# Optimization experiments

Measured on AMD Instinct MI355X. Metric: run time of the kernel, lower is better.

Reference implementation:

```python
import jax, jax.numpy as jnp
import numpy as np

SCALE = 0.05  # temperature from the module
C, NUM, IN_DIM, HID = 64, 128, 768, 128


def _l2norm(x):
    n = jnp.sqrt(jnp.sum(x * x, axis=-1, keepdims=True))
    return x / jnp.maximum(n, 1e-12)


def setup_inputs() -> dict:
    key = jax.random.key(0)
    k1, k2, k3, k4 = jax.random.split(key, 4)
    embeds = jax.random.normal(k1, (C, NUM, IN_DIM), dtype=jnp.float32)
    head_w = jax.random.normal(k2, (HID, IN_DIM), dtype=jnp.float32) * (1.0 / np.sqrt(IN_DIM))
    head_b = jax.random.normal(k3, (HID,), dtype=jnp.float32) * 0.01
    proto = jax.random.normal(k4, (C, HID), dtype=jnp.float32) * (1.0 / np.sqrt(HID))
    return {"embeds": embeds, "head_w": head_w, "head_b": head_b, "proto": proto}


def reference(embeds, head_w, head_b, proto):
    # x = head(embeds): [C, num, hid]
    x = jnp.einsum('cni,hi->cnh', embeds, head_w) + head_b
    num = x.shape[1]
    num_classes = proto.shape[0]

    nx = _l2norm(x)            # [C, num, d]
    nproto = _l2norm(proto)    # [C, d]

    # ---- prototype contrastive term (loop over i in num, fused) ----
    # sim_mat[c, n, k] = exp(cos(x[c,n], proto[k]) / scale)
    sim_mat = jnp.exp(jnp.einsum('cnd,kd->cnk', nx, nproto) / SCALE)
    pos = jnp.diagonal(sim_mat, axis1=0, axis2=2)      # [num, C], pos[n,c] = sim_mat[c,n,c]
    total = sim_mat.sum(-1).T                           # [num, C]
    loss = -jnp.log(pos / total).sum()
    loss = loss / (num * num_classes * num_classes)

    # ---- instance-instance term (loop over i in num_classes, fused) ----
    # S[a, m, b, n] = exp(cos(x[a,m], x[b,n]) / scale)
    S = jnp.exp(jnp.einsum('amd,bnd->ambn', nx, nx) / SCALE)
    # per-anchor-class i: pos_ins[m, n] = S[i, m, i, n]
    pos_ins = jnp.diagonal(S, axis1=0, axis2=2)         # [m, n, C(i)]
    sumA = jnp.transpose(S.sum(0), (0, 2, 1))           # [m, n, C(i)]
    neg_ins = (sumA - pos_ins).sum(0)                   # [n, C(i)]
    loss_ins = -jnp.log(pos_ins / (pos_ins + neg_ins[None, :, :])).sum()
    loss_ins = loss_ins / (num * num_classes * num * num_classes)

    return loss + loss_ins
```

## Files before the change

### kernel.cpp

```cpp
#include <hip/hip_runtime.h>
#include <math.h>

#define SCALE_INV 20.0f
#define EXPK 28.853900817779268f
#define LN2F 0.6931471805599453f

typedef __bf16 bf16x8 __attribute__((ext_vector_type(8)));
typedef float  f32x4  __attribute__((ext_vector_type(4)));

__global__ __launch_bounds__(256) void k_prep(const float* __restrict__ w,
                                              const float* __restrict__ proto,
                                              __bf16* __restrict__ wb,
                                              __bf16* __restrict__ nprE,
                                              float* __restrict__ accs) {
  const int b = blockIdx.x, t = threadIdx.x;
  if (b < 32) {
    __shared__ float wsum[4];
    const int sub = t >> 7, tt = t & 127, row = b * 2 + sub;
    float v = proto[row * 128 + tt];
    float s = v * v;
    for (int off = 32; off; off >>= 1) s += __shfl_xor(s, off, 64);
    if ((t & 63) == 0) wsum[t >> 6] = s;
    __syncthreads();
    float inv = 1.0f / fmaxf(sqrtf(wsum[sub * 2] + wsum[sub * 2 + 1]), 1e-12f);
    nprE[row * 128 + tt] = (__bf16)(v * inv * EXPK);
    if (b == 0 && t < 4) accs[t] = 0.0f;
  } else {
    int i = (b - 32) * 1024 + t * 4;
    float4 f = *(const float4*)&w[i];
    __bf16 o[4] = {(__bf16)f.x, (__bf16)f.y, (__bf16)f.z, (__bf16)f.w};
    *(float*)&wb[i] = *(float*)o;
  }
}

__global__ __launch_bounds__(256) void k_headnorm(const float* __restrict__ e,
                                                  const __bf16* __restrict__ wb,
                                                  const float* __restrict__ hb,
                                                  __bf16* __restrict__ nxb,
                                                  __bf16* __restrict__ nxe) {
  __shared__ __bf16 Ab[32 * 136];
  __shared__ __bf16 Bb[128 * 136];
  __shared__ float  xt[32 * 132];
  __shared__ float  hbl[128];
  const int t  = threadIdx.x;
  const int rt = blockIdx.x;
  if (t < 128) hbl[t] = hb[t];

  const int arow = t >> 3, akoff = (t & 7) * 16;
  const int brow = t >> 1, bkoff = (t & 1) * 64;
  float4 ar[4];
  bf16x8 brg[8];
  {
    const float* p = &e[(rt * 32 + arow) * 768 + akoff];
    for (int i = 0; i < 4; i++) ar[i] = *(const float4*)(p + 4 * i);
    const __bf16* q = &wb[brow * 768 + bkoff];
    for (int i = 0; i < 8; i++) brg[i] = *(const bf16x8*)(q + 8 * i);
  }

  const int wv = t >> 6, lane = t & 63;
  const int quad = lane >> 4, lrow = lane & 15;
  const int rb = wv & 1, cb = wv >> 1;
  f32x4 acc[4];
  f32x4 zero = {0.f, 0.f, 0.f, 0.f};
  for (int j = 0; j < 4; j++) acc[j] = zero;

  for (int it = 0; it < 6; it++) {
    {
      __bf16 ta[16];
      const float* f = (const float*)ar;
      for (int i = 0; i < 16; i++) ta[i] = (__bf16)f[i];
      *(bf16x8*)&Ab[arow * 136 + akoff]     = *(bf16x8*)ta;
      *(bf16x8*)&Ab[arow * 136 + akoff + 8] = *(bf16x8*)(ta + 8);
      for (int seg = 0; seg < 8; seg++)
        *(bf16x8*)&Bb[brow * 136 + bkoff + seg * 8] = brg[seg];
    }
    __syncthreads();
    if (it < 5) {
      int kb = (it + 1) * 128;
      const float* p = &e[(rt * 32 + arow) * 768 + kb + akoff];
      for (int i = 0; i < 4; i++) ar[i] = *(const float4*)(p + 4 * i);
      const __bf16* q = &wb[brow * 768 + kb + bkoff];
      for (int i = 0; i < 8; i++) brg[i] = *(const bf16x8*)(q + 8 * i);
    }
    for (int kc = 0; kc < 4; kc++) {
      bf16x8 a = *(const bf16x8*)&Ab[(rb * 16 + lrow) * 136 + kc * 32 + quad * 8];
      for (int j = 0; j < 4; j++) {
        bf16x8 b = *(const bf16x8*)&Bb[(cb * 64 + j * 16 + lrow) * 136 + kc * 32 + quad * 8];
        acc[j] = __builtin_amdgcn_mfma_f32_16x16x32_bf16(a, b, acc[j], 0, 0, 0);
      }
    }
    __syncthreads();
  }

  for (int j = 0; j < 4; j++)
    for (int r = 0; r < 4; r++) {
      int row = rb * 16 + quad * 4 + r;
      int col = cb * 64 + j * 16 + lrow;
      xt[row * 132 + col] = acc[j][r] + hbl[col];
    }
  __syncthreads();
  {
    int row = t >> 3, c0 = (t & 7) * 16;
    float v[16];
    float s = 0.0f;
    for (int i = 0; i < 4; i++) {
      float4 f = *(const float4*)&xt[row * 132 + c0 + i * 4];
      v[i * 4] = f.x; v[i * 4 + 1] = f.y; v[i * 4 + 2] = f.z; v[i * 4 + 3] = f.w;
    }
    for (int i = 0; i < 16; i++) s += v[i] * v[i];
    s += __shfl_xor(s, 1, 64);
    s += __shfl_xor(s, 2, 64);
    s += __shfl_xor(s, 4, 64);
    float inv = 1.0f / fmaxf(sqrtf(s), 1e-12f);
    __bf16 o[16], oe[16];
    for (int i = 0; i < 16; i++) {
      float nv = v[i] * inv;
      o[i]  = (__bf16)nv;
      oe[i] = (__bf16)(nv * EXPK);
    }
    __bf16* dst = &nxb[(rt * 32 + row) * 128 + c0];
    *(bf16x8*)dst       = *(bf16x8*)o;
    *(bf16x8*)(dst + 8) = *(bf16x8*)(o + 8);
    __bf16* dse = &nxe[(rt * 32 + row) * 128 + c0];
    *(bf16x8*)dse       = *(bf16x8*)oe;
    *(bf16x8*)(dse + 8) = *(bf16x8*)(oe + 8);
  }
}

__global__ __launch_bounds__(256) void k_colsum(const __bf16* __restrict__ nxb,
                                                const __bf16* __restrict__ nxe,
                                                float* __restrict__ cspart) {
  __shared__ __bf16 At[128 * 136];
  __shared__ __bf16 Bt[128 * 136];
  __shared__ float  colpart[4 * 128];
  const int t    = threadIdx.x;
  const int ct   = blockIdx.x;
  const int rs   = blockIdx.y;
  const int w    = t >> 6, lane = t & 63;
  const int quad = lane >> 4, lrow = lane & 15;
  const int sr   = t >> 4, sseg = t & 15;

  for (int it = 0; it < 8; it++) {
    int r = sr + it * 16;
    *(bf16x8*)&Bt[r * 136 + sseg * 8] =
        *(const bf16x8*)&nxe[(ct * 128 + r) * 128 + sseg * 8];
  }
  int tiles[8], nt = 0;
  for (int c8 = 0; c8 < 8; c8++) {
    int row0 = rs * 1024 + c8 * 128;
    if (row0 != ct * 128) tiles[nt++] = row0;
  }
  bf16x8 pre[8];
  for (int it = 0; it < 8; it++)
    pre[it] = *(const bf16x8*)&nxb[(tiles[0] + sr + it * 16) * 128 + sseg * 8];

  float colacc[8];
  for (int j = 0; j < 8; j++) colacc[j] = 0.0f;

  for (int ti = 0; ti < nt; ti++) {
    for (int it = 0; it < 8; it++)
      *(bf16x8*)&At[(sr + it * 16) * 136 + sseg * 8] = pre[it];
    __syncthreads();
    if (ti + 1 < nt) {
      int row0 = tiles[ti + 1];
      for (int it = 0; it < 8; it++)
        pre[it] = *(const bf16x8*)&nxb[(row0 + sr + it * 16) * 128 + sseg * 8];
    }
    f32x4 acc[2][8];
    f32x4 zero = {0.0f, 0.0f, 0.0f, 0.0f};
    for (int i = 0; i < 2; i++)
      for (int j = 0; j < 8; j++) acc[i][j] = zero;
    for (int kc = 0; kc < 4; kc++) {
      bf16x8 a0 = *(const bf16x8*)&At[(w * 32 + lrow) * 136 + kc * 32 + quad * 8];
      bf16x8 a1 = *(const bf16x8*)&At[(w * 32 + 16 + lrow) * 136 + kc * 32 + quad * 8];
      for (int j = 0; j < 8; j++) {
        bf16x8 b = *(const bf16x8*)&Bt[(j * 16 + lrow) * 136 + kc * 32 + quad * 8];
        acc[0][j] = __builtin_amdgcn_mfma_f32_16x16x32_bf16(a0, b, acc[0][j], 0, 0, 0);
        acc[1][j] = __builtin_amdgcn_mfma_f32_16x16x32_bf16(a1, b, acc[1][j], 0, 0, 0);
      }
    }
    for (int i = 0; i < 2; i++)
      for (int j = 0; j < 8; j++)
        for (int r = 0; r < 4; r++)
          colacc[j] += exp2f(acc[i][j][r]);
    __syncthreads();
  }

  for (int j = 0; j < 8; j++) {
    float v = colacc[j];
    v += __shfl_xor(v, 16, 64);
    v += __shfl_xor(v, 32, 64);
    if (lane < 16) colpart[w * 128 + j * 16 + lane] = v;
  }
  __syncthreads();
  if (t < 128) {
    float s = colpart[t] + colpart[128 + t] + colpart[256 + t] + colpart[384 + t];
    cspart[rs * 8192 + ct * 128 + t] = s;
  }
}

__global__ __launch_bounds__(256) void k_fused(const __bf16* __restrict__ nxb,
                                               const __bf16* __restrict__ nxe,
                                               const __bf16* __restrict__ nprE,
                                               const float* __restrict__ cspart,
                                               float* __restrict__ accs,
                                               float* __restrict__ out) {
  __shared__ __bf16 Xt[64 * 136];
  __shared__ __bf16 XtE[128 * 136];
  __shared__ __bf16 PtE[64 * 136];
  __shared__ float  negl[128];
  const int t = threadIdx.x, cls = blockIdx.x, half = blockIdx.y;
  const int sr = t >> 4, sseg = t & 15;

  for (int it = 0; it < 4; it++) {
    int r = sr + it * 16;
    *(bf16x8*)&Xt[r * 136 + sseg * 8] =
        *(const bf16x8*)&nxb[(cls * 128 + half * 64 + r) * 128 + sseg * 8];
    *(bf16x8*)&PtE[r * 136 + sseg * 8] =
        *(const bf16x8*)&nprE[r * 128 + sseg * 8];
  }
  for (int it = 0; it < 8; it++) {
    int r = sr + it * 16;
    *(bf16x8*)&XtE[r * 136 + sseg * 8] =
        *(const bf16x8*)&nxe[(cls * 128 + r) * 128 + sseg * 8];
  }
  if (t < 128) {
    float s = 0.0f;
    for (int s8 = 0; s8 < 8; s8++) s += cspart[s8 * 8192 + cls * 128 + t];
    negl[t] = s;
  }
  __syncthreads();

  const int wv = t >> 6, lane = t & 63;
  const int quad = lane >> 4, lrow = lane & 15;
  f32x4 zero = {0.f, 0.f, 0.f, 0.f};
  f32x4 acc_i[8], acc_p[4];
  for (int j = 0; j < 8; j++) acc_i[j] = zero;
  for (int j = 0; j < 4; j++) acc_p[j] = zero;

  for (int kc = 0; kc < 4; kc++) {
    bf16x8 a = *(const bf16x8*)&Xt[(wv * 16 + lrow) * 136 + kc * 32 + quad * 8];
    for (int j = 0; j < 8; j++) {
      bf16x8 b = *(const bf16x8*)&XtE[(j * 16 + lrow) * 136 + kc * 32 + quad * 8];
      acc_i[j] = __builtin_amdgcn_mfma_f32_16x16x32_bf16(a, b, acc_i[j], 0, 0, 0);
    }
    for (int j = 0; j < 4; j++) {
      bf16x8 b = *(const bf16x8*)&PtE[(j * 16 + lrow) * 136 + kc * 32 + quad * 8];
      acc_p[j] = __builtin_amdgcn_mfma_f32_16x16x32_bf16(a, b, acc_p[j], 0, 0, 0);
    }
  }

  float wacc0 = 0.0f;
  for (int r = 0; r < 4; r++) {
    float tot = 0.0f;
    for (int j = 0; j < 4; j++) tot += exp2f(acc_p[j][r]);
    tot += __shfl_xor(tot, 1, 64);
    tot += __shfl_xor(tot, 2, 64);
    tot += __shfl_xor(tot, 4, 64);
    tot += __shfl_xor(tot, 8, 64);
    if (lrow == 0) wacc0 += logf(tot);
  }
  {
    const int jc = cls >> 4, colc = cls & 15;
    if (lrow == colc) {
      float sd = 0.0f;
      switch (jc) {
        case 0: for (int r = 0; r < 4; r++) sd += acc_p[0][r]; break;
        case 1: for (int r = 0; r < 4; r++) sd += acc_p[1][r]; break;
        case 2: for (int r = 0; r < 4; r++) sd += acc_p[2][r]; break;
        default: for (int r = 0; r < 4; r++) sd += acc_p[3][r]; break;
      }
      wacc0 -= sd * LN2F;
    }
  }
  float wacc1 = 0.0f;
  for (int j = 0; j < 8; j++) {
    float ng = negl[j * 16 + lrow];
    for (int r = 0; r < 4; r++)
      wacc1 += log1pf(ng * exp2f(-acc_i[j][r]));
  }
  for (int off = 32; off; off >>= 1) {
    wacc0 += __shfl_xor(wacc0, off, 64);
    wacc1 += __shfl_xor(wacc1, off, 64);
  }
  if (lane == 0) {
    atomicAdd(&accs[0], wacc0);
    atomicAdd(&accs[1], wacc1);
  }
  __syncthreads();
  if (t == 0) {
    __threadfence();
    unsigned int old = atomicAdd((unsigned int*)&accs[2], 1u);
    if (old == 127u) {
      __threadfence();
      float a0 = atomicAdd(&accs[0], 0.0f);
      float a1 = atomicAdd(&accs[1], 0.0f);
      out[0] = a0 * (1.0f / 524288.0f) + a1 * (1.0f / 67108864.0f);
    }
  }
}

extern "C" void kernel_launch(void* const* d_in, const int* in_sizes, int n_in,
                              void* d_out, int out_size, void* d_ws, size_t ws_size,
                              hipStream_t stream) {
  const float* e  = (const float*)d_in[0];
  const float* w  = (const float*)d_in[1];
  const float* hb = (const float*)d_in[2];
  const float* pr = (const float*)d_in[3];
  char* ws = (char*)d_ws;
  __bf16* nxb    = (__bf16*)ws;
  __bf16* nxe    = (__bf16*)(ws + (2 << 20));
  __bf16* wb     = (__bf16*)(ws + (4 << 20));
  __bf16* nprE   = (__bf16*)(ws + (4 << 20) + (256 << 10));
  float*  cspart = (float*)(ws + (4 << 20) + (512 << 10));
  float*  accs   = (float*)(ws + (5 << 20));
  float*  out    = (float*)d_out;

  k_prep<<<128, 256, 0, stream>>>(w, pr, wb, nprE, accs);
  k_headnorm<<<256, 256, 0, stream>>>(e, wb, hb, nxb, nxe);
  k_colsum<<<dim3(64, 8), 256, 0, stream>>>(nxb, nxe, cspart);
  k_fused<<<dim3(64, 2), 256, 0, stream>>>(nxb, nxe, nprE, cspart, accs, out);
}
```

Before: 152.1 us.

## Exploit Gram symmetry in colsum, drop prep kernel, fuse weight/proto conversion

The column-sum kernel now computes each off-diagonal class-pair tile only once. It accumulates both column sums and row sums, via shuffles and atomics, into a single cspart buffer, which halves the exp-heavy MFMA work. The k_prep launch is removed: head weights are converted from fp32 to bf16 on the fly inside k_headnorm, using a 64-wide k-step, and prototype normalization moves into k_fused. This trades extra global atomics and redundant per-block proto normalization for fewer tiles and one fewer launch.

```diff
diff --git a/kernel.cpp b/kernel.cpp
--- a/kernel.cpp
+++ b/kernel.cpp
@@ -8,53 +8,31 @@
 typedef __bf16 bf16x8 __attribute__((ext_vector_type(8)));
 typedef float  f32x4  __attribute__((ext_vector_type(4)));
 
-__global__ __launch_bounds__(256) void k_prep(const float* __restrict__ w,
-                                              const float* __restrict__ proto,
-                                              __bf16* __restrict__ wb,
-                                              __bf16* __restrict__ nprE,
-                                              float* __restrict__ accs) {
-  const int b = blockIdx.x, t = threadIdx.x;
-  if (b < 32) {
-    __shared__ float wsum[4];
-    const int sub = t >> 7, tt = t & 127, row = b * 2 + sub;
-    float v = proto[row * 128 + tt];
-    float s = v * v;
-    for (int off = 32; off; off >>= 1) s += __shfl_xor(s, off, 64);
-    if ((t & 63) == 0) wsum[t >> 6] = s;
-    __syncthreads();
-    float inv = 1.0f / fmaxf(sqrtf(wsum[sub * 2] + wsum[sub * 2 + 1]), 1e-12f);
-    nprE[row * 128 + tt] = (__bf16)(v * inv * EXPK);
-    if (b == 0 && t < 4) accs[t] = 0.0f;
-  } else {
-    int i = (b - 32) * 1024 + t * 4;
-    float4 f = *(const float4*)&w[i];
-    __bf16 o[4] = {(__bf16)f.x, (__bf16)f.y, (__bf16)f.z, (__bf16)f.w};
-    *(float*)&wb[i] = *(float*)o;
-  }
-}
-
 __global__ __launch_bounds__(256) void k_headnorm(const float* __restrict__ e,
-                                                  const __bf16* __restrict__ wb,
+                                                  const float* __restrict__ w,
                                                   const float* __restrict__ hb,
                                                   __bf16* __restrict__ nxb,
-                                                  __bf16* __restrict__ nxe) {
-  __shared__ __bf16 Ab[32 * 136];
-  __shared__ __bf16 Bb[128 * 136];
+                                                  __bf16* __restrict__ nxe,
+                                                  float* __restrict__ cspart,
+                                                  float* __restrict__ accs) {
+  __shared__ __bf16 Ab[32 * 72];
+  __shared__ __bf16 Bb[128 * 72];
   __shared__ float  xt[32 * 132];
   __shared__ float  hbl[128];
   const int t  = threadIdx.x;
   const int rt = blockIdx.x;
   if (t < 128) hbl[t] = hb[t];
-
-  const int arow = t >> 3, akoff = (t & 7) * 16;
-  const int brow = t >> 1, bkoff = (t & 1) * 64;
-  float4 ar[4];
-  bf16x8 brg[8];
+  if (t < 32) cspart[rt * 32 + t] = 0.0f;
+  if (rt == 0 && t >= 128 && t < 132) accs[t - 128] = 0.0f;
+
+  const int arow = t >> 3, akoff = (t & 7) * 8;
+  const int brow = t >> 1, bkoff = (t & 1) * 32;
+  float4 ar[2], br[8];
   {
     const float* p = &e[(rt * 32 + arow) * 768 + akoff];
-    for (int i = 0; i < 4; i++) ar[i] = *(const float4*)(p + 4 * i);
-    const __bf16* q = &wb[brow * 768 + bkoff];
-    for (int i = 0; i < 8; i++) brg[i] = *(const bf16x8*)(q + 8 * i);
+    ar[0] = *(const float4*)p; ar[1] = *(const float4*)(p + 4);
+    const float* q = &w[brow * 768 + bkoff];
+    for (int i = 0; i < 8; i++) br[i] = *(const float4*)(q + 4 * i);
   }
 
   const int wv = t >> 6, lane = t & 63;
@@ -64,28 +42,31 @@
   f32x4 zero = {0.f, 0.f, 0.f, 0.f};
   for (int j = 0; j < 4; j++) acc[j] = zero;
 
-  for (int it = 0; it < 6; it++) {
+  for (int it = 0; it < 12; it++) {
     {
-      __bf16 ta[16];
+      __bf16 ta[8];
       const float* f = (const float*)ar;
-      for (int i = 0; i < 16; i++) ta[i] = (__bf16)f[i];
-      *(bf16x8*)&Ab[arow * 136 + akoff]     = *(bf16x8*)ta;
-      *(bf16x8*)&Ab[arow * 136 + akoff + 8] = *(bf16x8*)(ta + 8);
-      for (int seg = 0; seg < 8; seg++)
-        *(bf16x8*)&Bb[brow * 136 + bkoff + seg * 8] = brg[seg];
+      for (int i = 0; i < 8; i++) ta[i] = (__bf16)f[i];
+      *(bf16x8*)&Ab[arow * 72 + akoff] = *(bf16x8*)ta;
+      const float* g = (const float*)br;
+      for (int seg = 0; seg < 4; seg++) {
+        __bf16 tb[8];
+        for (int i = 0; i < 8; i++) tb[i] = (__bf16)g[seg * 8 + i];
+        *(bf16x8*)&Bb[brow * 72 + bkoff + seg * 8] = *(bf16x8*)tb;
+      }
     }
     __syncthreads();
-    if (it < 5) {
-      int kb = (it + 1) * 128;
+    if (it < 11) {
+      int kb = (it + 1) * 64;
       const float* p = &e[(rt * 32 + arow) * 768 + kb + akoff];
-      for (int i = 0; i < 4; i++) ar[i] = *(const float4*)(p + 4 * i);
-      const __bf16* q = &wb[brow * 768 + kb + bkoff];
-      for (int i = 0; i < 8; i++) brg[i] = *(const bf16x8*)(q + 8 * i);
-    }
-    for (int kc = 0; kc < 4; kc++) {
-      bf16x8 a = *(const bf16x8*)&Ab[(rb * 16 + lrow) * 136 + kc * 32 + quad * 8];
+      ar[0] = *(const float4*)p; ar[1] = *(const float4*)(p + 4);
+      const float* q = &w[brow * 768 + kb + bkoff];
+      for (int i = 0; i < 8; i++) br[i] = *(const float4*)(q + 4 * i);
+    }
+    for (int kc = 0; kc < 2; kc++) {
+      bf16x8 a = *(const bf16x8*)&Ab[(rb * 16 + lrow) * 72 + kc * 32 + quad * 8];
       for (int j = 0; j < 4; j++) {
-        bf16x8 b = *(const bf16x8*)&Bb[(cb * 64 + j * 16 + lrow) * 136 + kc * 32 + quad * 8];
+        bf16x8 b = *(const bf16x8*)&Bb[(cb * 64 + j * 16 + lrow) * 72 + kc * 32 + quad * 8];
         acc[j] = __builtin_amdgcn_mfma_f32_16x16x32_bf16(a, b, acc[j], 0, 0, 0);
       }
     }
@@ -134,7 +115,7 @@
   __shared__ __bf16 Bt[128 * 136];
   __shared__ float  colpart[4 * 128];
   const int t    = threadIdx.x;
-  const int ct   = blockIdx.x;
+  const int cj   = blockIdx.x;
   const int rs   = blockIdx.y;
   const int w    = t >> 6, lane = t & 63;
   const int quad = lane >> 4, lrow = lane & 15;
@@ -143,28 +124,29 @@
   for (int it = 0; it < 8; it++) {
     int r = sr + it * 16;
     *(bf16x8*)&Bt[r * 136 + sseg * 8] =
-        *(const bf16x8*)&nxe[(ct * 128 + r) * 128 + sseg * 8];
-  }
-  int tiles[8], nt = 0;
-  for (int c8 = 0; c8 < 8; c8++) {
-    int row0 = rs * 1024 + c8 * 128;
-    if (row0 != ct * 128) tiles[nt++] = row0;
+        *(const bf16x8*)&nxe[(cj * 128 + r) * 128 + sseg * 8];
+  }
+  int tiles[4], nt = 0;
+  for (int mm = 0; mm < 4; mm++) {
+    int m = rs * 4 + 1 + mm;
+    if (m < 32 || cj < 32) tiles[nt++] = (cj + m) & 63;
   }
   bf16x8 pre[8];
   for (int it = 0; it < 8; it++)
-    pre[it] = *(const bf16x8*)&nxb[(tiles[0] + sr + it * 16) * 128 + sseg * 8];
+    pre[it] = *(const bf16x8*)&nxb[(tiles[0] * 128 + sr + it * 16) * 128 + sseg * 8];
 
   float colacc[8];
   for (int j = 0; j < 8; j++) colacc[j] = 0.0f;
 
   for (int ti = 0; ti < nt; ti++) {
+    const int ci = tiles[ti];
     for (int it = 0; it < 8; it++)
       *(bf16x8*)&At[(sr + it * 16) * 136 + sseg * 8] = pre[it];
     __syncthreads();
     if (ti + 1 < nt) {
-      int row0 = tiles[ti + 1];
+      int cn = tiles[ti + 1];
       for (int it = 0; it < 8; it++)
-        pre[it] = *(const bf16x8*)&nxb[(row0 + sr + it * 16) * 128 + sseg * 8];
+        pre[it] = *(const bf16x8*)&nxb[(cn * 128 + sr + it * 16) * 128 + sseg * 8];
     }
     f32x4 acc[2][8];
     f32x4 zero = {0.0f, 0.0f, 0.0f, 0.0f};
@@ -179,10 +161,26 @@
         acc[1][j] = __builtin_amdgcn_mfma_f32_16x16x32_bf16(a1, b, acc[1][j], 0, 0, 0);
       }
     }
+    float rsum[2][4];
+    for (int i = 0; i < 2; i++)
+      for (int r = 0; r < 4; r++) rsum[i][r] = 0.0f;
     for (int i = 0; i < 2; i++)
       for (int j = 0; j < 8; j++)
-        for (int r = 0; r < 4; r++)
-          colacc[j] += exp2f(acc[i][j][r]);
+        for (int r = 0; r < 4; r++) {
+          float ev = exp2f(acc[i][j][r]);
+          colacc[j]  += ev;
+          rsum[i][r] += ev;
+        }
+    for (int i = 0; i < 2; i++)
+      for (int r = 0; r < 4; r++) {
+        float v = rsum[i][r];
+        v += __shfl_xor(v, 1, 64);
+        v += __shfl_xor(v, 2, 64);
+        v += __shfl_xor(v, 4, 64);
+        v += __shfl_xor(v, 8, 64);
+        if (lrow == 0)
+          atomicAdd(&cspart[ci * 128 + w * 32 + i * 16 + quad * 4 + r], v);
+      }
     __syncthreads();
   }
 
@@ -195,13 +193,13 @@
   __syncthreads();
   if (t < 128) {
     float s = colpart[t] + colpart[128 + t] + colpart[256 + t] + colpart[384 + t];
-    cspart[rs * 8192 + ct * 128 + t] = s;
+    atomicAdd(&cspart[cj * 128 + t], s);
   }
 }
 
 __global__ __launch_bounds__(256) void k_fused(const __bf16* __restrict__ nxb,
                                                const __bf16* __restrict__ nxe,
-                                               const __bf16* __restrict__ nprE,
+                                               const float* __restrict__ proto,
                                                const float* __restrict__ cspart,
                                                float* __restrict__ accs,
                                                float* __restrict__ out) {
@@ -212,23 +210,35 @@
   const int t = threadIdx.x, cls = blockIdx.x, half = blockIdx.y;
   const int sr = t >> 4, sseg = t & 15;
 
+  {
+    const int rw = t >> 2, part = t & 3;
+    float v[32];
+    float s = 0.0f;
+    const float* p = &proto[rw * 128 + part * 32];
+    for (int i = 0; i < 8; i++) {
+      float4 f = *(const float4*)(p + 4 * i);
+      v[i * 4] = f.x; v[i * 4 + 1] = f.y; v[i * 4 + 2] = f.z; v[i * 4 + 3] = f.w;
+      s += f.x * f.x + f.y * f.y + f.z * f.z + f.w * f.w;
+    }
+    s += __shfl_xor(s, 1, 64);
+    s += __shfl_xor(s, 2, 64);
+    float inv = EXPK / fmaxf(sqrtf(s), 1e-12f);
+    __bf16 o[32];
+    for (int i = 0; i < 32; i++) o[i] = (__bf16)(v[i] * inv);
+    __bf16* dst = &PtE[rw * 136 + part * 32];
+    for (int i = 0; i < 4; i++) *(bf16x8*)(dst + i * 8) = *(bf16x8*)(o + i * 8);
+  }
   for (int it = 0; it < 4; it++) {
     int r = sr + it * 16;
     *(bf16x8*)&Xt[r * 136 + sseg * 8] =
         *(const bf16x8*)&nxb[(cls * 128 + half * 64 + r) * 128 + sseg * 8];
-    *(bf16x8*)&PtE[r * 136 + sseg * 8] =
-        *(const bf16x8*)&nprE[r * 128 + sseg * 8];
   }
   for (int it = 0; it < 8; it++) {
     int r = sr + it * 16;
     *(bf16x8*)&XtE[r * 136 + sseg * 8] =
         *(const bf16x8*)&nxe[(cls * 128 + r) * 128 + sseg * 8];
   }
-  if (t < 128) {
-    float s = 0.0f;
-    for (int s8 = 0; s8 < 8; s8++) s += cspart[s8 * 8192 + cls * 128 + t];
-    negl[t] = s;
-  }
+  if (t < 128) negl[t] = cspart[cls * 128 + t];
   __syncthreads();
 
   const int wv = t >> 6, lane = t & 63;
@@ -310,14 +320,11 @@
   char* ws = (char*)d_ws;
   __bf16* nxb    = (__bf16*)ws;
   __bf16* nxe    = (__bf16*)(ws + (2 << 20));
-  __bf16* wb     = (__bf16*)(ws + (4 << 20));
-  __bf16* nprE   = (__bf16*)(ws + (4 << 20) + (256 << 10));
-  float*  cspart = (float*)(ws + (4 << 20) + (512 << 10));
-  float*  accs   = (float*)(ws + (5 << 20));
+  float*  cspart = (float*)(ws + (4 << 20));
+  float*  accs   = (float*)(ws + (4 << 20) + (64 << 10));
   float*  out    = (float*)d_out;
 
-  k_prep<<<128, 256, 0, stream>>>(w, pr, wb, nprE, accs);
-  k_headnorm<<<256, 256, 0, stream>>>(e, wb, hb, nxb, nxe);
+  k_headnorm<<<256, 256, 0, stream>>>(e, w, hb, nxb, nxe, cspart, accs);
   k_colsum<<<dim3(64, 8), 256, 0, stream>>>(nxb, nxe, cspart);
-  k_fused<<<dim3(64, 2), 256, 0, stream>>>(nxb, nxe, nprE, cspart, accs, out);
+  k_fused<<<dim3(64, 2), 256, 0, stream>>>(nxb, nxe, pr, cspart, accs, out);
 }
```

New measurement: 142.0 us. 6.6% less time.
